# Kernel optimization log

Measured on AMD Instinct MI355X. Metric: run time of the kernel, lower is better.

Reference implementation:

```python
import jax, jax.numpy as jnp
import numpy as np

B, L, V = 8192, 64, 28
LATENT = 32
PAD_TOKEN, EOS_TOKEN = 26, 27
EPS = 1e-7
LETTER_FREQS = jnp.array([0.0817, 0.0149, 0.0278, 0.0425, 0.127, 0.0223, 0.0202,
                          0.0609, 0.0697, 0.0015, 0.0077, 0.0403, 0.0241, 0.0675,
                          0.0751, 0.0193, 0.001, 0.0599, 0.0633, 0.0906, 0.0276,
                          0.0098, 0.0236, 0.0015, 0.0197, 0.0007], dtype=jnp.float32)
FREQS_PAD = jnp.pad(LETTER_FREQS, (0, V - 26))  # tf.pad to VOCAB_SIZE


def setup_inputs() -> dict:
    key = jax.random.key(0)
    k1, k2, k3, k4, k5 = jax.random.split(key, 5)
    x = jax.random.normal(k1, (B, L, V), dtype=jnp.float32)
    # decoder output is a softmax -> valid probability tensor
    reconstruction = jax.nn.softmax(jax.random.normal(k2, (B, L, V), dtype=jnp.float32), axis=-1)
    z_mean = jax.random.normal(k3, (B, LATENT), dtype=jnp.float32)
    z_log_var = jax.random.normal(k4, (B, LATENT), dtype=jnp.float32)
    classifier_score = jax.random.uniform(k5, (B, 1), dtype=jnp.float32)
    return {"x": x, "reconstruction": reconstruction, "z_mean": z_mean,
            "z_log_var": z_log_var, "classifier_score": classifier_score}


def _total_loss(x, reconstruction, z_mean, z_log_var, classifier_score):
    targets = jnp.argmax(x, axis=-1)                       # [B, L] int
    mask = (targets != PAD_TOKEN).astype(jnp.float32)      # [B, L]

    # sparse categorical CE on probabilities (tf clips probs)
    p_tgt = jnp.take_along_axis(reconstruction, targets[..., None], axis=-1)[..., 0]
    per_position_loss = -jnp.log(jnp.clip(p_tgt, EPS, 1.0))
    reconstruction_loss = jnp.sum(per_position_loss * mask) / jnp.sum(mask)

    kl_loss = -0.5 * jnp.mean(1.0 + z_log_var - jnp.square(z_mean) - jnp.exp(z_log_var))

    classifier_loss = -jnp.mean(jnp.log(classifier_score + EPS))

    # consecutive similarity: sum_i i^2.5 * sum_j prod(adjacent[:, j:j+i])
    mask_adj = (targets[:, 1:] != PAD_TOKEN).astype(jnp.float32)       # [B, L-1]
    adjacent = jnp.sum(reconstruction[:, 1:] * reconstruction[:, :-1], axis=-1) * mask_adj
    Lm1 = L - 1
    pos = jnp.arange(Lm1)

    def step(carry, k):
        # k = i - 1; p[:, j] holds prod(adjacent[:, j:j+k]) from previous step
        p, acc = carry
        valid = (pos < (Lm1 - k)).astype(adjacent.dtype)               # [L-1]
        shifted = jnp.roll(adjacent, -k, axis=1) * valid               # adjacent[:, j+k], 0 past end
        p = p * shifted                                                # window length k+1; invalid j -> 0
        w = jnp.power((k + 1).astype(jnp.float32), 2.5)
        acc = acc + w * jnp.sum(p)
        return (p, acc), None

    init = (adjacent, jnp.sum(adjacent))                               # i = 1, weight 1^2.5
    (_, consecutive_similarity), _ = jax.lax.scan(step, init, jnp.arange(1, Lm1))

    mask_exp = jnp.logical_and(targets != PAD_TOKEN, targets != EOS_TOKEN).astype(jnp.float32)[:, :, None]
    mean_letter_probs = jnp.sum(reconstruction * mask_exp, axis=(0, 1)) / jnp.sum(mask_exp)
    frequency_penalty = jnp.sum(jnp.maximum(0.0, mean_letter_probs - FREQS_PAD))

    total_loss = (reconstruction_loss + 0.1 * kl_loss + 2.0 * classifier_loss
                  + 0.2 * consecutive_similarity + 0.5 * frequency_penalty)
    return total_loss


def reference(x, reconstruction, z_mean, z_log_var, classifier_score):
    return _total_loss(x, reconstruction, z_mean, z_log_var, classifier_score)
```

## Files before the change

### kernel.cpp

```cpp
#include <hip/hip_runtime.h>
#include <math.h>

#define VB 28
#define LL 64
#define PAD_TOK 26
#define EOS_TOK 27
#define NSLOT 34
#define REPL 8

constexpr double csqrt_(double x) {
  double g = x > 1.0 ? x : 1.0;
  for (int i = 0; i < 60; ++i) g = 0.5 * (g + x / g);
  return g;
}
struct WTab { float w[64]; };
constexpr WTab make_wtab() {
  WTab t{};
  for (int k = 0; k < 64; ++k) {
    double n = (double)(k + 1);
    t.w[k] = (float)(n * n * csqrt_(n));
  }
  return t;
}
constexpr WTab WTAB = make_wtab();

__device__ __forceinline__ float wave_red(float v) {
  #pragma unroll
  for (int o = 32; o > 0; o >>= 1) v += __shfl_down(v, o, 64);
  return v;
}

__global__ __launch_bounds__(256) void vae_main(
    const float* __restrict__ x, const float* __restrict__ rec,
    const float* __restrict__ zm, const float* __restrict__ zlv,
    const float* __restrict__ cs, float* __restrict__ ws,
    int nrows, int nz, int nc, int nblocks) {
  __shared__ float adj_s[4][128];
  __shared__ float red[4][NSLOT];
  const int lane = threadIdx.x & 63;
  const int wid  = threadIdx.x >> 6;
  adj_s[wid][64 + lane] = 0.f;
  __builtin_amdgcn_wave_barrier();

  float loss_acc = 0.f, mask_cnt = 0.f, mexp_cnt = 0.f;
  float consec0 = 0.f, consec1 = 0.f;
  float vocab[VB];
  #pragma unroll
  for (int v = 0; v < VB; ++v) vocab[v] = 0.f;

  const int wave_id = blockIdx.x * 4 + wid;
  const int n_waves = nblocks * 4;

  for (int row = wave_id; row < nrows; row += n_waves) {
    const size_t base = ((size_t)row * LL + lane) * VB;
    const float4* xp = reinterpret_cast<const float4*>(x + base);
    const float4* rp = reinterpret_cast<const float4*>(rec + base);
    float r[VB];
    float best = -INFINITY, pt = 0.f;
    int tgt = 0;
    #pragma unroll
    for (int i = 0; i < 7; ++i) {
      float4 xq = xp[i];
      float4 rq = rp[i];
      r[i*4+0] = rq.x; r[i*4+1] = rq.y; r[i*4+2] = rq.z; r[i*4+3] = rq.w;
      if (xq.x > best) { best = xq.x; tgt = i*4+0; pt = rq.x; }
      if (xq.y > best) { best = xq.y; tgt = i*4+1; pt = rq.y; }
      if (xq.z > best) { best = xq.z; tgt = i*4+2; pt = rq.z; }
      if (xq.w > best) { best = xq.w; tgt = i*4+3; pt = rq.w; }
    }
    const float mask = (tgt != PAD_TOK) ? 1.f : 0.f;
    const float mexp = (tgt != PAD_TOK && tgt != EOS_TOK) ? 1.f : 0.f;
    loss_acc += -__logf(fminf(fmaxf(pt, 1e-7f), 1.f)) * mask;
    mask_cnt += mask;
    mexp_cnt += mexp;
    #pragma unroll
    for (int v = 0; v < VB; ++v) vocab[v] += r[v] * mexp;

    float adj = 0.f;
    #pragma unroll
    for (int v = 0; v < VB; ++v) adj += r[v] * __shfl_down(r[v], 1, 64);
    const int tgt_next = __shfl_down(tgt, 1, 64);
    adj = (lane < 63 && tgt_next != PAD_TOK) ? adj : 0.f;

    __builtin_amdgcn_wave_barrier();
    adj_s[wid][lane] = adj;
    __builtin_amdgcn_wave_barrier();

    const float* ap = &adj_s[wid][lane];
    float p = adj;
    consec0 += p;
    #pragma unroll
    for (int k = 1; k <= 62; k += 2) {
      p *= ap[k];
      consec1 += WTAB.w[k] * p;
      if (k + 1 <= 62) {
        p *= ap[k + 1];
        consec0 += WTAB.w[k + 1] * p;
      }
    }
    __builtin_amdgcn_wave_barrier();
  }
  float consec_acc = consec0 + consec1;

  const int gid = blockIdx.x * 256 + threadIdx.x;
  const int gstride = nblocks * 256;
  float kl = 0.f, cl = 0.f;
  for (int i = gid; i < nz; i += gstride) {
    const float m = zm[i], lv = zlv[i];
    kl += 1.f + lv - m * m - __expf(lv);
  }
  for (int i = gid; i < nc; i += gstride) cl += __logf(cs[i] + 1e-7f);

  loss_acc   = wave_red(loss_acc);
  mask_cnt   = wave_red(mask_cnt);
  consec_acc = wave_red(consec_acc);
  mexp_cnt   = wave_red(mexp_cnt);
  kl         = wave_red(kl);
  cl         = wave_red(cl);
  #pragma unroll
  for (int v = 0; v < VB; ++v) vocab[v] = wave_red(vocab[v]);

  if (lane == 0) {
    red[wid][0] = loss_acc; red[wid][1] = mask_cnt;
    red[wid][2] = consec_acc; red[wid][3] = mexp_cnt;
    red[wid][4] = kl; red[wid][5] = cl;
    #pragma unroll
    for (int v = 0; v < VB; ++v) red[wid][6 + v] = vocab[v];
  }
  __syncthreads();
  if (threadIdx.x < NSLOT) {
    const int t = threadIdx.x;
    float* bank = ws + ((blockIdx.x & (REPL - 1)) << 6);
    atomicAdd(&bank[t], red[0][t] + red[1][t] + red[2][t] + red[3][t]);
  }
}

__global__ void vae_finalize(const float* __restrict__ ws, float* __restrict__ out,
                             float nz, float nc) {
  if (threadIdx.x == 0 && blockIdx.x == 0) {
    const float freqs[VB] = {0.0817f,0.0149f,0.0278f,0.0425f,0.127f,0.0223f,
      0.0202f,0.0609f,0.0697f,0.0015f,0.0077f,0.0403f,0.0241f,0.0675f,0.0751f,
      0.0193f,0.001f,0.0599f,0.0633f,0.0906f,0.0276f,0.0098f,0.0236f,0.0015f,
      0.0197f,0.0007f,0.f,0.f};
    float fin[NSLOT];
    #pragma unroll
    for (int t = 0; t < NSLOT; ++t) {
      float s = 0.f;
      #pragma unroll
      for (int b = 0; b < REPL; ++b) s += ws[(b << 6) + t];
      fin[t] = s;
    }
    const float rec_loss = fin[0] / fin[1];
    const float kl_loss  = -0.5f * fin[4] / nz;
    const float cls_loss = -fin[5] / nc;
    const float inv_mexp = 1.f / fin[3];
    float fp = 0.f;
    #pragma unroll
    for (int v = 0; v < VB; ++v)
      fp += fmaxf(0.f, fin[6 + v] * inv_mexp - freqs[v]);
    out[0] = rec_loss + 0.1f * kl_loss + 2.f * cls_loss
           + 0.2f * fin[2] + 0.5f * fp;
  }
}

extern "C" void kernel_launch(void* const* d_in, const int* in_sizes, int n_in,
                              void* d_out, int out_size, void* d_ws, size_t ws_size,
                              hipStream_t stream) {
  const float* x   = (const float*)d_in[0];
  const float* rec = (const float*)d_in[1];
  const float* zm  = (const float*)d_in[2];
  const float* zlv = (const float*)d_in[3];
  const float* cs  = (const float*)d_in[4];
  float* out = (float*)d_out;
  float* ws  = (float*)d_ws;

  const int nrows = in_sizes[0] / (LL * VB);
  const int nz    = in_sizes[2];
  const int nc    = in_sizes[4];

  int nblocks = (nrows + 3) / 4;
  if (nblocks < 1) nblocks = 1;

  hipMemsetAsync(d_ws, 0, REPL * 64 * sizeof(float), stream);
  vae_main<<<nblocks, 256, 0, stream>>>(x, rec, zm, zlv, cs, ws,
                                        nrows, nz, nc, nblocks);
  vae_finalize<<<1, 64, 0, stream>>>(ws, out, (float)nz, (float)nc);
}
```

Before: 180.9 us.

## Process four rows per wave with register prefetch and spread atomic slots

Each wave now handles four consecutive rows and loads the next row's x and reconstruction data into registers while computing the current row, with a quarter as many blocks launched. The workspace atomics are spread so each slot and replica bank sits 32 floats apart, reducing same-cache-line atomic contention. A launch-bounds occupancy hint of 2 is added. Prefetch buffers double register use for the loaded data, and fewer blocks means fewer waves in flight to hide memory latency.

New measurement: 157.4 us. 1.15x faster.

```diff
diff --git a/kernel.cpp b/kernel.cpp
--- a/kernel.cpp
+++ b/kernel.cpp
@@ -7,6 +7,7 @@
 #define EOS_TOK 27
 #define NSLOT 34
 #define REPL 8
+#define RPW 4
 
 constexpr double csqrt_(double x) {
   double g = x > 1.0 ? x : 1.0;
@@ -30,7 +31,7 @@
   return v;
 }
 
-__global__ __launch_bounds__(256) void vae_main(
+__global__ __launch_bounds__(256, 2) void vae_main(
     const float* __restrict__ x, const float* __restrict__ rec,
     const float* __restrict__ zm, const float* __restrict__ zlv,
     const float* __restrict__ cs, float* __restrict__ ws,
@@ -49,19 +50,43 @@
   for (int v = 0; v < VB; ++v) vocab[v] = 0.f;
 
   const int wave_id = blockIdx.x * 4 + wid;
-  const int n_waves = nblocks * 4;
-
-  for (int row = wave_id; row < nrows; row += n_waves) {
-    const size_t base = ((size_t)row * LL + lane) * VB;
-    const float4* xp = reinterpret_cast<const float4*>(x + base);
-    const float4* rp = reinterpret_cast<const float4*>(rec + base);
+  const int row0 = wave_id * RPW;
+
+  float4 xa[7], ra[7];
+  {
+    const int row = row0;
+    if (row < nrows) {
+      const size_t base = ((size_t)row * LL + lane) * VB;
+      const float4* xp = reinterpret_cast<const float4*>(x + base);
+      const float4* rp = reinterpret_cast<const float4*>(rec + base);
+      #pragma unroll
+      for (int i = 0; i < 7; ++i) { xa[i] = xp[i]; ra[i] = rp[i]; }
+    }
+  }
+
+  #pragma unroll
+  for (int it = 0; it < RPW; ++it) {
+    const int row = row0 + it;
+    if (row >= nrows) break;
+
+    float4 xb[7], rb[7];
+    const int nrow = row + 1;
+    const bool pf = (it + 1 < RPW) && (nrow < nrows);
+    if (pf) {
+      const size_t base = ((size_t)nrow * LL + lane) * VB;
+      const float4* xp = reinterpret_cast<const float4*>(x + base);
+      const float4* rp = reinterpret_cast<const float4*>(rec + base);
+      #pragma unroll
+      for (int i = 0; i < 7; ++i) { xb[i] = xp[i]; rb[i] = rp[i]; }
+    }
+
     float r[VB];
     float best = -INFINITY, pt = 0.f;
     int tgt = 0;
     #pragma unroll
     for (int i = 0; i < 7; ++i) {
-      float4 xq = xp[i];
-      float4 rq = rp[i];
+      const float4 xq = xa[i];
+      const float4 rq = ra[i];
       r[i*4+0] = rq.x; r[i*4+1] = rq.y; r[i*4+2] = rq.z; r[i*4+3] = rq.w;
       if (xq.x > best) { best = xq.x; tgt = i*4+0; pt = rq.x; }
       if (xq.y > best) { best = xq.y; tgt = i*4+1; pt = rq.y; }
@@ -99,6 +124,11 @@
       }
     }
     __builtin_amdgcn_wave_barrier();
+
+    if (pf) {
+      #pragma unroll
+      for (int i = 0; i < 7; ++i) { xa[i] = xb[i]; ra[i] = rb[i]; }
+    }
   }
   float consec_acc = consec0 + consec1;
 
@@ -130,8 +160,9 @@
   __syncthreads();
   if (threadIdx.x < NSLOT) {
     const int t = threadIdx.x;
-    float* bank = ws + ((blockIdx.x & (REPL - 1)) << 6);
-    atomicAdd(&bank[t], red[0][t] + red[1][t] + red[2][t] + red[3][t]);
+    const int b = blockIdx.x & (REPL - 1);
+    atomicAdd(&ws[t * (REPL * 32) + b * 32],
+              red[0][t] + red[1][t] + red[2][t] + red[3][t]);
   }
 }
 
@@ -147,7 +178,7 @@
     for (int t = 0; t < NSLOT; ++t) {
       float s = 0.f;
       #pragma unroll
-      for (int b = 0; b < REPL; ++b) s += ws[(b << 6) + t];
+      for (int b = 0; b < REPL; ++b) s += ws[t * (REPL * 32) + b * 32];
       fin[t] = s;
     }
     const float rec_loss = fin[0] / fin[1];
@@ -178,10 +209,10 @@
   const int nz    = in_sizes[2];
   const int nc    = in_sizes[4];
 
-  int nblocks = (nrows + 3) / 4;
+  int nblocks = (nrows + 4 * RPW - 1) / (4 * RPW);
   if (nblocks < 1) nblocks = 1;
 
-  hipMemsetAsync(d_ws, 0, REPL * 64 * sizeof(float), stream);
+  hipMemsetAsync(d_ws, 0, NSLOT * REPL * 32 * sizeof(float), stream);
   vae_main<<<nblocks, 256, 0, stream>>>(x, rec, zm, zlv, cs, ws,
                                         nrows, nz, nc, nblocks);
   vae_finalize<<<1, 64, 0, stream>>>(ws, out, (float)nz, (float)nc);
```
